# Kernel optimization log

Hardware: AMD Instinct MI355X
Metric: run time of the kernel (lower is better)

## Reference

```python
import jax, jax.numpy as jnp
from jax import lax
import numpy as np

KERNEL = 3
PAD = KERNEL // 2


def _normalized_weights(affinity):
    # affinity: [B, 8, H, W] -> 9-tap weights [B, 9, H, W] with center at index 4
    aff_sum = jnp.sum(jnp.abs(affinity), axis=1, keepdims=True)
    aff_norm = affinity / aff_sum
    center = 1.0 - jnp.sum(aff_norm, axis=1, keepdims=True)
    # Original loop uses affinity channels 0..3 for taps before center, 4..7 after
    return jnp.concatenate([aff_norm[:, :4], center, aff_norm[:, 4:]], axis=1)


def setup_inputs() -> dict:
    key = jax.random.key(0)
    k1, k2 = jax.random.split(key)
    B, H, W = 8, 480, 640
    affinity = jax.random.normal(k1, (B, KERNEL * KERNEL - 1, H, W), dtype=jnp.float32)
    feature = jax.random.normal(k2, (B, 1, H, W), dtype=jnp.float32)
    return {"affinity": affinity, "feature": feature, "times": 24}


def reference(affinity, feature, times):
    weights = _normalized_weights(affinity)  # [B, 9, H, W]
    B, C, H, W = feature.shape

    def step(f, _):
        fp = jnp.pad(f, ((0, 0), (0, 0), (PAD, PAD), (PAD, PAD)))
        # 9 shifted views stacked on a tap axis: [B, 9, C, H, W]
        shifts = jnp.stack(
            [fp[:, :, i:i + H, j:j + W] for i in range(KERNEL) for j in range(KERNEL)],
            axis=1,
        )
        f_new = jnp.sum(shifts * weights[:, :, None, :, :], axis=1)
        return f_new, None

    out, _ = lax.scan(step, feature, None, length=times)
    return out
```

## Files before the change

kernel.cpp:

```cpp
#include <hip/hip_runtime.h>
#include <hip/hip_fp16.h>
#include <cstddef>


#define HIMG 480
#define WIMG 640
#define HW   (HIMG * WIMG)
#define BN   8

#define TILE   40
#define TSTEPS 12
#define IH     13
#define WHL    12
#define SW     66
#define PITCH  68
#define NT     512

#define WS_FRAME_B  ((size_t)BN * HW * 4)
#define WS_WA_B     ((size_t)BN * HW * 16)
#define WS_WC_B     ((size_t)BN * HW * 4)
#define WS_NEED     (WS_FRAME_B + WS_WA_B + WS_WC_B)

template <int MODE>
__global__ __launch_bounds__(NT, 4) void affprop12(
    const float* __restrict__ aff,
    __half2* __restrict__ wA,
    float* __restrict__ wC,
    const float* __restrict__ src,
    float* __restrict__ dst)
{
    __shared__ float fA[SW * PITCH];
    __shared__ float fB[SW * PITCH];

    const int tid = threadIdx.x;
    const int ox  = blockIdx.x * TILE;
    const int oy  = blockIdx.y * TILE;
    const int b   = blockIdx.z;

    const float* __restrict__ sb = src + (size_t)b * HW;
    float*       __restrict__ db = dst + (size_t)b * HW;

    for (int i = tid; i < SW * SW; i += NT) {
        int r  = i / SW;
        int c  = i - r * SW;
        int gy = oy - IH + r;
        int gx = ox - IH + c;
        float v = 0.f;
        if ((unsigned)gy < (unsigned)HIMG && (unsigned)gx < (unsigned)WIMG)
            v = sb[gy * WIMG + gx];
        fA[r * PITCH + c] = v;
    }
    for (int i = tid; i < SW * PITCH / 4; i += NT)
        *(float4*)&fB[4 * i] = make_float4(0.f, 0.f, 0.f, 0.f);

    const int cu = tid & 31;
    const int rg = tid >> 5;
    const int w  = tid >> 6;

    __half2 wv[4][2][4];
    float   wcc[4][2];

    #pragma unroll
    for (int i = 0; i < 4; ++i) {
        #pragma unroll
        for (int k = 0; k < 2; ++k) {
            const int gy = oy - WHL + 4 * rg + i;
            const int gx = ox - WHL + 2 * cu + k;
            const bool in = (unsigned)gy < (unsigned)HIMG && (unsigned)gx < (unsigned)WIMG;
            const size_t idx = (size_t)b * HW + (size_t)gy * WIMG + gx;

            if (MODE == 1) {
                if (in) {
                    union { float4 f4; __half2 h[4]; } u;
                    u.f4 = *(const float4*)(wA + 4 * idx);
                    wv[i][k][0] = u.h[0]; wv[i][k][1] = u.h[1];
                    wv[i][k][2] = u.h[2]; wv[i][k][3] = u.h[3];
                    wcc[i][k] = wC[idx];
                } else {
                    __half2 z = __floats2half2_rn(0.f, 0.f);
                    wv[i][k][0] = z; wv[i][k][1] = z;
                    wv[i][k][2] = z; wv[i][k][3] = z;
                    wcc[i][k] = 0.f;
                }
            } else {
                float wt[8];
                float s = 0.f;
                if (in) {
                    const float* ap = aff + (size_t)b * 8 * HW + (size_t)gy * WIMG + gx;
                    #pragma unroll
                    for (int t = 0; t < 8; ++t) { wt[t] = ap[(size_t)t * HW]; s += fabsf(wt[t]); }
                } else {
                    #pragma unroll
                    for (int t = 0; t < 8; ++t) wt[t] = 0.f;
                    s = 1.f;
                }
                float rr  = in ? 1.0f / s : 0.f;
                float acc = 0.f;
                #pragma unroll
                for (int t = 0; t < 8; ++t) { wt[t] *= rr; acc += wt[t]; }

                union { float4 f4; __half2 h[4]; } u;
                u.h[0] = __floats2half2_rn(wt[0], wt[1]);
                u.h[1] = __floats2half2_rn(wt[2], wt[3]);
                u.h[2] = __floats2half2_rn(wt[4], wt[5]);
                u.h[3] = __floats2half2_rn(wt[6], wt[7]);
                wv[i][k][0] = u.h[0]; wv[i][k][1] = u.h[1];
                wv[i][k][2] = u.h[2]; wv[i][k][3] = u.h[3];
                wcc[i][k] = in ? 1.0f - acc : 0.f;

                if (MODE == 0) {
                    if ((unsigned)(gy - oy) < (unsigned)TILE &&
                        (unsigned)(gx - ox) < (unsigned)TILE) {
                        *(float4*)(wA + 4 * idx) = u.f4;
                        wC[idx] = wcc[i][k];
                    }
                }
            }
        }
    }
    __syncthreads();

    const float* fin = fA;
    float*       fo  = fB;

    #pragma unroll 1
    for (int s = 0; s < TSTEPS; ++s) {
        const bool live = (8 * w + 8 >= s + 1) && (8 * w + 1 <= 64 - s);
        if (live) {
            const float* bp = fin + (4 * rg) * PITCH + 2 * cu;
            float2 p0[6], p1[6];
            #pragma unroll
            for (int r = 0; r < 6; ++r) {
                p0[r] = *(const float2*)(bp + r * PITCH);
                p1[r] = *(const float2*)(bp + r * PITCH + 2);
            }
            float Wm[6][4];
            #pragma unroll
            for (int r = 0; r < 6; ++r) {
                Wm[r][0] = p0[r].x; Wm[r][1] = p0[r].y;
                Wm[r][2] = p1[r].x; Wm[r][3] = p1[r].y;
            }
            float* wp = fo + (4 * rg + 1) * PITCH + (2 * cu + 1);
            #pragma unroll
            for (int i = 0; i < 4; ++i) {
                #pragma unroll
                for (int k = 0; k < 2; ++k) {
                    float o = wcc[i][k] * Wm[i + 1][k + 1]
                        + __low2float (wv[i][k][0]) * Wm[i][k]
                        + __high2float(wv[i][k][0]) * Wm[i][k + 1]
                        + __low2float (wv[i][k][1]) * Wm[i][k + 2]
                        + __high2float(wv[i][k][1]) * Wm[i + 1][k]
                        + __low2float (wv[i][k][2]) * Wm[i + 1][k + 2]
                        + __high2float(wv[i][k][2]) * Wm[i + 2][k]
                        + __low2float (wv[i][k][3]) * Wm[i + 2][k + 1]
                        + __high2float(wv[i][k][3]) * Wm[i + 2][k + 2];
                    wp[i * PITCH + k] = o;
                }
            }
        }
        __syncthreads();
        const float* t = fin; fin = fo; fo = (float*)t;
    }

    for (int i = tid; i < TILE * (TILE / 4); i += NT) {
        int r  = i / (TILE / 4);
        int c4 = (i - r * (TILE / 4)) * 4;
        const float* p = fin + (IH + r) * PITCH + IH + c4;
        float4 v = make_float4(p[0], p[1], p[2], p[3]);
        *(float4*)&db[(size_t)(oy + r) * WIMG + ox + c4] = v;
    }
}

extern "C" void kernel_launch(void* const* d_in, const int* in_sizes, int n_in,
                              void* d_out, int out_size, void* d_ws, size_t ws_size,
                              hipStream_t stream)
{
    const float* aff  = (const float*)d_in[0];
    const float* feat = (const float*)d_in[1];
    float* out = (float*)d_out;

    char* ws = (char*)d_ws;
    float*   wsFrame = (float*)ws;
    __half2* wA      = (__half2*)(ws + WS_FRAME_B);
    float*   wC      = (float*)(ws + WS_FRAME_B + WS_WA_B);

    dim3 blk(NT, 1, 1);
    dim3 grd(WIMG / TILE, HIMG / TILE, BN);

    if (ws_size >= WS_NEED) {
        affprop12<0><<<grd, blk, 0, stream>>>(aff, wA, wC, feat, wsFrame);
        affprop12<1><<<grd, blk, 0, stream>>>(aff, wA, wC, wsFrame, out);
    } else {
        affprop12<2><<<grd, blk, 0, stream>>>(aff, nullptr, nullptr, feat, wsFrame);
        affprop12<2><<<grd, blk, 0, stream>>>(aff, nullptr, nullptr, wsFrame, out);
    }
}
```

Before: 232.4 us.

## Remap threads to 2x4 output patches with float4 LDS reads and shifted halo

Each thread now computes a 2-row by 4-column output patch instead of 4x2. The shared tile is shifted by one column so that reads are 16-byte aligned float4 loads and writes are float2 stores, which cuts the number of LDS instructions per step. The occupancy hint in launch bounds is raised from 4 to 6, which pressures register allocation. It also changes which threads are live per wave at each step, and it risks LDS bank conflicts with the new access stride.

```diff
diff --git a/kernel.cpp b/kernel.cpp
--- a/kernel.cpp
+++ b/kernel.cpp
@@ -12,7 +12,7 @@
 #define TSTEPS 12
 #define IH     13
 #define WHL    12
-#define SW     66
+#define ROWS   66
 #define PITCH  68
 #define NT     512
 
@@ -22,15 +22,15 @@
 #define WS_NEED     (WS_FRAME_B + WS_WA_B + WS_WC_B)
 
 template <int MODE>
-__global__ __launch_bounds__(NT, 4) void affprop12(
+__global__ __launch_bounds__(NT, 6) void affprop12(
     const float* __restrict__ aff,
     __half2* __restrict__ wA,
     float* __restrict__ wC,
     const float* __restrict__ src,
     float* __restrict__ dst)
 {
-    __shared__ float fA[SW * PITCH];
-    __shared__ float fB[SW * PITCH];
+    __shared__ float fA[ROWS * PITCH];
+    __shared__ float fB[ROWS * PITCH];
 
     const int tid = threadIdx.x;
     const int ox  = blockIdx.x * TILE;
@@ -40,32 +40,32 @@
     const float* __restrict__ sb = src + (size_t)b * HW;
     float*       __restrict__ db = dst + (size_t)b * HW;
 
-    for (int i = tid; i < SW * SW; i += NT) {
-        int r  = i / SW;
-        int c  = i - r * SW;
+    for (int i = tid; i < ROWS * PITCH; i += NT) {
+        int r  = i / PITCH;
+        int c  = i - r * PITCH;
         int gy = oy - IH + r;
-        int gx = ox - IH + c;
+        int gx = ox - IH - 1 + c;
         float v = 0.f;
         if ((unsigned)gy < (unsigned)HIMG && (unsigned)gx < (unsigned)WIMG)
             v = sb[gy * WIMG + gx];
-        fA[r * PITCH + c] = v;
-    }
-    for (int i = tid; i < SW * PITCH / 4; i += NT)
+        fA[i] = v;
+    }
+    for (int i = tid; i < ROWS * PITCH / 4; i += NT)
         *(float4*)&fB[4 * i] = make_float4(0.f, 0.f, 0.f, 0.f);
 
-    const int cu = tid & 31;
-    const int rg = tid >> 5;
+    const int cu = tid & 15;
+    const int R  = tid >> 4;
     const int w  = tid >> 6;
 
-    __half2 wv[4][2][4];
-    float   wcc[4][2];
+    __half2 wv[2][4][4];
+    float   wcc[2][4];
 
     #pragma unroll
-    for (int i = 0; i < 4; ++i) {
+    for (int r = 0; r < 2; ++r) {
         #pragma unroll
-        for (int k = 0; k < 2; ++k) {
-            const int gy = oy - WHL + 4 * rg + i;
-            const int gx = ox - WHL + 2 * cu + k;
+        for (int k = 0; k < 4; ++k) {
+            const int gy = oy - WHL + 2 * R + r;
+            const int gx = ox - WHL + 4 * cu + k;
             const bool in = (unsigned)gy < (unsigned)HIMG && (unsigned)gx < (unsigned)WIMG;
             const size_t idx = (size_t)b * HW + (size_t)gy * WIMG + gx;
 
@@ -73,14 +73,14 @@
                 if (in) {
                     union { float4 f4; __half2 h[4]; } u;
                     u.f4 = *(const float4*)(wA + 4 * idx);
-                    wv[i][k][0] = u.h[0]; wv[i][k][1] = u.h[1];
-                    wv[i][k][2] = u.h[2]; wv[i][k][3] = u.h[3];
-                    wcc[i][k] = wC[idx];
+                    wv[r][k][0] = u.h[0]; wv[r][k][1] = u.h[1];
+                    wv[r][k][2] = u.h[2]; wv[r][k][3] = u.h[3];
+                    wcc[r][k] = wC[idx];
                 } else {
                     __half2 z = __floats2half2_rn(0.f, 0.f);
-                    wv[i][k][0] = z; wv[i][k][1] = z;
-                    wv[i][k][2] = z; wv[i][k][3] = z;
-                    wcc[i][k] = 0.f;
+                    wv[r][k][0] = z; wv[r][k][1] = z;
+                    wv[r][k][2] = z; wv[r][k][3] = z;
+                    wcc[r][k] = 0.f;
                 }
             } else {
                 float wt[8];
@@ -104,15 +104,15 @@
                 u.h[1] = __floats2half2_rn(wt[2], wt[3]);
                 u.h[2] = __floats2half2_rn(wt[4], wt[5]);
                 u.h[3] = __floats2half2_rn(wt[6], wt[7]);
-                wv[i][k][0] = u.h[0]; wv[i][k][1] = u.h[1];
-                wv[i][k][2] = u.h[2]; wv[i][k][3] = u.h[3];
-                wcc[i][k] = in ? 1.0f - acc : 0.f;
+                wv[r][k][0] = u.h[0]; wv[r][k][1] = u.h[1];
+                wv[r][k][2] = u.h[2]; wv[r][k][3] = u.h[3];
+                wcc[r][k] = in ? 1.0f - acc : 0.f;
 
                 if (MODE == 0) {
                     if ((unsigned)(gy - oy) < (unsigned)TILE &&
                         (unsigned)(gx - ox) < (unsigned)TILE) {
                         *(float4*)(wA + 4 * idx) = u.f4;
-                        wC[idx] = wcc[i][k];
+                        wC[idx] = wcc[r][k];
                     }
                 }
             }
@@ -127,36 +127,47 @@
     for (int s = 0; s < TSTEPS; ++s) {
         const bool live = (8 * w + 8 >= s + 1) && (8 * w + 1 <= 64 - s);
         if (live) {
-            const float* bp = fin + (4 * rg) * PITCH + 2 * cu;
-            float2 p0[6], p1[6];
+            const float* bp = fin + (2 * R) * PITCH + 4 * cu;
+            float4 A0 = *(const float4*)(bp);
+            float4 A1 = *(const float4*)(bp + 4);
+            float4 B0 = *(const float4*)(bp + PITCH);
+            float4 B1 = *(const float4*)(bp + PITCH + 4);
+            float4 C0 = *(const float4*)(bp + 2 * PITCH);
+            float4 C1 = *(const float4*)(bp + 2 * PITCH + 4);
+            float4 D0 = *(const float4*)(bp + 3 * PITCH);
+            float4 D1 = *(const float4*)(bp + 3 * PITCH + 4);
+            float a[8] = {A0.x, A0.y, A0.z, A0.w, A1.x, A1.y, A1.z, A1.w};
+            float bb[8] = {B0.x, B0.y, B0.z, B0.w, B1.x, B1.y, B1.z, B1.w};
+            float cc[8] = {C0.x, C0.y, C0.z, C0.w, C1.x, C1.y, C1.z, C1.w};
+            float dd[8] = {D0.x, D0.y, D0.z, D0.w, D1.x, D1.y, D1.z, D1.w};
+
+            float o0[4], o1[4];
             #pragma unroll
-            for (int r = 0; r < 6; ++r) {
-                p0[r] = *(const float2*)(bp + r * PITCH);
-                p1[r] = *(const float2*)(bp + r * PITCH + 2);
+            for (int k = 0; k < 4; ++k) {
+                o0[k] = wcc[0][k] * bb[k + 2]
+                    + __low2float (wv[0][k][0]) * a [k + 1]
+                    + __high2float(wv[0][k][0]) * a [k + 2]
+                    + __low2float (wv[0][k][1]) * a [k + 3]
+                    + __high2float(wv[0][k][1]) * bb[k + 1]
+                    + __low2float (wv[0][k][2]) * bb[k + 3]
+                    + __high2float(wv[0][k][2]) * cc[k + 1]
+                    + __low2float (wv[0][k][3]) * cc[k + 2]
+                    + __high2float(wv[0][k][3]) * cc[k + 3];
+                o1[k] = wcc[1][k] * cc[k + 2]
+                    + __low2float (wv[1][k][0]) * bb[k + 1]
+                    + __high2float(wv[1][k][0]) * bb[k + 2]
+                    + __low2float (wv[1][k][1]) * bb[k + 3]
+                    + __high2float(wv[1][k][1]) * cc[k + 1]
+                    + __low2float (wv[1][k][2]) * cc[k + 3]
+                    + __high2float(wv[1][k][2]) * dd[k + 1]
+                    + __low2float (wv[1][k][3]) * dd[k + 2]
+                    + __high2float(wv[1][k][3]) * dd[k + 3];
             }
-            float Wm[6][4];
-            #pragma unroll
-            for (int r = 0; r < 6; ++r) {
-                Wm[r][0] = p0[r].x; Wm[r][1] = p0[r].y;
-                Wm[r][2] = p1[r].x; Wm[r][3] = p1[r].y;
-            }
-            float* wp = fo + (4 * rg + 1) * PITCH + (2 * cu + 1);
-            #pragma unroll
-            for (int i = 0; i < 4; ++i) {
-                #pragma unroll
-                for (int k = 0; k < 2; ++k) {
-                    float o = wcc[i][k] * Wm[i + 1][k + 1]
-                        + __low2float (wv[i][k][0]) * Wm[i][k]
-                        + __high2float(wv[i][k][0]) * Wm[i][k + 1]
-                        + __low2float (wv[i][k][1]) * Wm[i][k + 2]
-                        + __high2float(wv[i][k][1]) * Wm[i + 1][k]
-                        + __low2float (wv[i][k][2]) * Wm[i + 1][k + 2]
-                        + __high2float(wv[i][k][2]) * Wm[i + 2][k]
-                        + __low2float (wv[i][k][3]) * Wm[i + 2][k + 1]
-                        + __high2float(wv[i][k][3]) * Wm[i + 2][k + 2];
-                    wp[i * PITCH + k] = o;
-                }
-            }
+            float* wp = fo + (2 * R + 1) * PITCH + 4 * cu + 2;
+            *(float2*)(wp)             = make_float2(o0[0], o0[1]);
+            *(float2*)(wp + 2)         = make_float2(o0[2], o0[3]);
+            *(float2*)(wp + PITCH)     = make_float2(o1[0], o1[1]);
+            *(float2*)(wp + PITCH + 2) = make_float2(o1[2], o1[3]);
         }
         __syncthreads();
         const float* t = fin; fin = fo; fo = (float*)t;
@@ -165,7 +176,7 @@
     for (int i = tid; i < TILE * (TILE / 4); i += NT) {
         int r  = i / (TILE / 4);
         int c4 = (i - r * (TILE / 4)) * 4;
-        const float* p = fin + (IH + r) * PITCH + IH + c4;
+        const float* p = fin + (IH + r) * PITCH + (IH + 1) + c4;
         float4 v = make_float4(p[0], p[1], p[2], p[3]);
         *(float4*)&db[(size_t)(oy + r) * WIMG + ox + c4] = v;
     }
```

Result: slower. 513.5 us (+120.9%).
